# Kernel optimization log

Hardware: AMD Instinct MI355X
Metric: run time of the kernel (lower is better)

## Reference

```python
import jax, jax.numpy as jnp
import numpy as np

N = 50000      # nodes
E = 800000     # edges (before self-loops)
F_IN = 256
H = 4          # heads
C1 = 128
C2 = 64
NCLS = 50
NEG_SLOPE = 0.2


def setup_inputs() -> dict:
    key = jax.random.key(0)
    ks = jax.random.split(key, 12)
    x = jax.random.normal(ks[0], (N, F_IN), dtype=jnp.float32)
    edge_index = jax.random.randint(ks[1], (2, E), 0, N, dtype=jnp.int32)
    s1 = 1.0 / np.sqrt(F_IN)
    s2 = 1.0 / np.sqrt(H * C1)
    s3 = 1.0 / np.sqrt(H * C2)
    return {
        "x": x,
        "edge_index": edge_index,
        "W1": jax.random.normal(ks[2], (F_IN, H * C1), dtype=jnp.float32) * s1,
        "a_src1": jax.random.normal(ks[3], (H, C1), dtype=jnp.float32) * s2,
        "a_dst1": jax.random.normal(ks[4], (H, C1), dtype=jnp.float32) * s2,
        "b1": jnp.zeros((H * C1,), dtype=jnp.float32),
        "W2": jax.random.normal(ks[5], (H * C1, H * C2), dtype=jnp.float32) * s2,
        "a_src2": jax.random.normal(ks[6], (H, C2), dtype=jnp.float32) * s3,
        "a_dst2": jax.random.normal(ks[7], (H, C2), dtype=jnp.float32) * s3,
        "b2": jnp.zeros((H * C2,), dtype=jnp.float32),
        "Wf": jax.random.normal(ks[8], (H * C2, NCLS), dtype=jnp.float32) * s3,
        "bf": jnp.zeros((NCLS,), dtype=jnp.float32),
    }


def _gat_conv(x, src, dst, W, a_src, a_dst, b, heads, ch):
    # h: [N, H, C] transformed features
    h = (x @ W).reshape(N, heads, ch)
    # per-node attention halves (standard GAT decomposition, avoids per-edge d-dim gather for scores)
    asrc = jnp.sum(h * a_src[None], axis=-1)  # [N, H]
    adst = jnp.sum(h * a_dst[None], axis=-1)  # [N, H]
    e = jax.nn.leaky_relu(asrc[src] + adst[dst], NEG_SLOPE)  # [E, H]
    # softmax over edges sharing the same destination node
    m = jax.ops.segment_max(e, dst, num_segments=N)          # [N, H]
    ex = jnp.exp(e - m[dst])
    denom = jax.ops.segment_sum(ex, dst, num_segments=N)     # [N, H]
    alpha = ex / (denom[dst] + 1e-16)                        # [E, H]
    msg = h[src] * alpha[:, :, None]                         # [E, H, C]
    out = jax.ops.segment_sum(msg, dst, num_segments=N)      # [N, H, C]
    return out.reshape(N, heads * ch) + b


def reference(x, edge_index, W1, a_src1, a_dst1, b1, W2, a_src2, a_dst2, b2, Wf, bf):
    # PyG GATConv adds self-loops by default
    loops = jnp.arange(N, dtype=edge_index.dtype)
    src = jnp.concatenate([edge_index[0], loops])
    dst = jnp.concatenate([edge_index[1], loops])
    h = _gat_conv(x, src, dst, W1, a_src1, a_dst1, b1, H, C1)
    h = jax.nn.elu(h)
    # F.dropout is identity in eval mode
    h = _gat_conv(h, src, dst, W2, a_src2, a_dst2, b2, H, C2)
    h = jax.nn.elu(h)
    return h @ Wf + bf
```

## Files before the change

kernel.cpp:

```cpp
#include <hip/hip_runtime.h>
#include <hip/hip_bf16.h>
#include <cmath>

#define NN 50000
#define EE 800000
#define ET 850000
#define HH 4
#define CC1 128
#define CC2 64
#define FIN 256
#define NCLS 50

typedef __attribute__((ext_vector_type(8))) short   short8;
typedef __attribute__((ext_vector_type(8))) unsigned short ushort8;
typedef __attribute__((ext_vector_type(4))) unsigned short ushortx4;
typedef __attribute__((ext_vector_type(4))) float   floatx4;

__device__ __forceinline__ unsigned short f2bf(float f) {
    union { float f; unsigned int u; } x; x.f = f;
    unsigned int lsb = (x.u >> 16) & 1u;
    x.u += 0x7fffu + lsb;
    return (unsigned short)(x.u >> 16);
}
__device__ __forceinline__ float bf2f(unsigned short b) {
    union { unsigned int u; float f; } x; x.u = ((unsigned int)b) << 16;
    return x.f;
}

typedef const __attribute__((address_space(1))) unsigned int* glds_gp_t;
typedef __attribute__((address_space(3))) unsigned int* glds_lp_t;
__device__ __forceinline__ void glds16(const void* g, void* l) {
    __builtin_amdgcn_global_load_lds((glds_gp_t)g, (glds_lp_t)l, 16, 0, 0);
}

__global__ __launch_bounds__(256) void cast_bf16(
    const float* __restrict__ in, unsigned short* __restrict__ out, int n4)
{
    int t = blockIdx.x * blockDim.x + threadIdx.x;
    if (t >= n4) return;
    float4 v = *(const float4*)(in + 4 * (size_t)t);
    unsigned short r0 = f2bf(v.x), r1 = f2bf(v.y), r2 = f2bf(v.z), r3 = f2bf(v.w);
    unsigned int lo = (unsigned int)r0 | ((unsigned int)r1 << 16);
    unsigned int hi = (unsigned int)r2 | ((unsigned int)r3 << 16);
    *(uint2*)(out + 4 * (size_t)t) = make_uint2(lo, hi);
}

__global__ __launch_bounds__(256) void transpose_cast(
    const float* __restrict__ W, unsigned short* __restrict__ Wt, int K, int N)
{
    int t = blockIdx.x * blockDim.x + threadIdx.x;
    if (t >= K * N) return;
    int n = t / K, k = t - n * K;
    Wt[t] = f2bf(W[(size_t)k * N + n]);
}

__global__ __launch_bounds__(256) void transpose_cast_pad(
    const float* __restrict__ W, unsigned short* __restrict__ Wt,
    int K, int N, int Npad)
{
    int t = blockIdx.x * blockDim.x + threadIdx.x;
    if (t >= K * Npad) return;
    int n = t / K, k = t - n * K;
    Wt[t] = (n < N) ? f2bf(W[(size_t)k * N + n]) : (unsigned short)0;
}

__global__ __launch_bounds__(256) void gemm_bf16_v2(
    const unsigned short* __restrict__ A,
    const unsigned short* __restrict__ Bt,
    unsigned short* __restrict__ C,
    int M, int N, int K)
{
    __shared__ unsigned short As[128 * 32];
    __shared__ unsigned short Bs[128 * 32];
    int tid = threadIdx.x, wave = tid >> 6, lane = tid & 63;
    int wm = (wave >> 1) * 64, wn = (wave & 1) * 64;
    int row0 = blockIdx.x * 128, col0 = blockIdx.y * 128;
    int lm = lane & 15, lq = lane >> 4, kq = lq * 8;
    floatx4 acc[4][4] = {};

    int srow = wave * 32 + (lane >> 2);
    int skk  = (lane & 3) * 8;
    int gra0 = row0 + srow;      if (gra0 >= M) gra0 = M - 1;
    int gra1 = row0 + srow + 16; if (gra1 >= M) gra1 = M - 1;
    const unsigned short* ga0 = A + (size_t)gra0 * K + skk;
    const unsigned short* ga1 = A + (size_t)gra1 * K + skk;
    const unsigned short* gb0 = Bt + (size_t)(col0 + srow) * K + skk;
    const unsigned short* gb1 = Bt + (size_t)(col0 + srow + 16) * K + skk;
    unsigned short* la0 = &As[(wave * 32) * 32];
    unsigned short* la1 = &As[(wave * 32 + 16) * 32];
    unsigned short* lb0 = &Bs[(wave * 32) * 32];
    unsigned short* lb1 = &Bs[(wave * 32 + 16) * 32];

    for (int k0 = 0; k0 < K; k0 += 32) {
        __syncthreads();
        glds16(ga0 + k0, la0);
        glds16(ga1 + k0, la1);
        glds16(gb0 + k0, lb0);
        glds16(gb1 + k0, lb1);
        __syncthreads();

        short8 af[4], bfr[4];
        #pragma unroll
        for (int mt = 0; mt < 4; ++mt)
            af[mt] = *(const short8*)&As[(wm + mt * 16 + lm) * 32 + kq];
        #pragma unroll
        for (int nt = 0; nt < 4; ++nt)
            bfr[nt] = *(const short8*)&Bs[(wn + nt * 16 + lm) * 32 + kq];
        #pragma unroll
        for (int mt = 0; mt < 4; ++mt)
            #pragma unroll
            for (int nt = 0; nt < 4; ++nt)
                acc[mt][nt] = __builtin_amdgcn_mfma_f32_16x16x32_bf16(
                    af[mt], bfr[nt], acc[mt][nt], 0, 0, 0);
    }

    #pragma unroll
    for (int mt = 0; mt < 4; ++mt) {
        int rbase = row0 + wm + mt * 16 + lq * 4;
        #pragma unroll
        for (int nt = 0; nt < 4; ++nt) {
            int c = col0 + wn + nt * 16 + lm;
            #pragma unroll
            for (int r = 0; r < 4; ++r) {
                int gr = rbase + r;
                if (gr < M) C[(size_t)gr * N + c] = f2bf(acc[mt][nt][r]);
            }
        }
    }
}

__global__ __launch_bounds__(128) void gemm_final(
    const unsigned short* __restrict__ A,
    const unsigned short* __restrict__ Bt,
    const float* __restrict__ bias,
    float* __restrict__ out, int M)
{
    __shared__ unsigned short As[128 * 40];
    __shared__ unsigned short Bs[64 * 40];
    int tid = threadIdx.x, wave = tid >> 6, lane = tid & 63;
    int row0 = blockIdx.x * 128;
    int lm = lane & 15, lq = lane >> 4, kq = lq * 8;
    floatx4 acc[4][4] = {};

    for (int k0 = 0; k0 < 256; k0 += 32) {
        int gr = row0 + tid; if (gr >= M) gr = M - 1;
        const unsigned short* ap = A + (size_t)gr * 256 + k0;
        ushort8 a0 = *(const ushort8*)ap;
        ushort8 a1 = *(const ushort8*)(ap + 8);
        ushort8 a2 = *(const ushort8*)(ap + 16);
        ushort8 a3 = *(const ushort8*)(ap + 24);
        const unsigned short* bp = Bt + (size_t)(tid >> 1) * 256 + k0 + (tid & 1) * 16;
        ushort8 b0 = *(const ushort8*)bp;
        ushort8 b1 = *(const ushort8*)(bp + 8);
        __syncthreads();
        *(ushort8*)&As[tid * 40 + 0]  = a0;
        *(ushort8*)&As[tid * 40 + 8]  = a1;
        *(ushort8*)&As[tid * 40 + 16] = a2;
        *(ushort8*)&As[tid * 40 + 24] = a3;
        *(ushort8*)&Bs[(tid >> 1) * 40 + (tid & 1) * 16]     = b0;
        *(ushort8*)&Bs[(tid >> 1) * 40 + (tid & 1) * 16 + 8] = b1;
        __syncthreads();

        short8 af[4], bfr[4];
        #pragma unroll
        for (int mt = 0; mt < 4; ++mt)
            af[mt] = *(const short8*)&As[(wave * 64 + mt * 16 + lm) * 40 + kq];
        #pragma unroll
        for (int nt = 0; nt < 4; ++nt)
            bfr[nt] = *(const short8*)&Bs[(nt * 16 + lm) * 40 + kq];
        #pragma unroll
        for (int mt = 0; mt < 4; ++mt)
            #pragma unroll
            for (int nt = 0; nt < 4; ++nt)
                acc[mt][nt] = __builtin_amdgcn_mfma_f32_16x16x32_bf16(
                    af[mt], bfr[nt], acc[mt][nt], 0, 0, 0);
    }

    #pragma unroll
    for (int mt = 0; mt < 4; ++mt) {
        int rbase = row0 + wave * 64 + mt * 16 + lq * 4;
        #pragma unroll
        for (int nt = 0; nt < 4; ++nt) {
            int c = nt * 16 + lm;
            if (c >= NCLS) continue;
            float bv = bias[c];
            #pragma unroll
            for (int r = 0; r < 4; ++r) {
                int gr = rbase + r;
                if (gr < M) out[(size_t)gr * NCLS + c] = acc[mt][nt][r] + bv;
            }
        }
    }
}

template<int C>
__global__ __launch_bounds__(256) void attn_scores2(
    const unsigned short* __restrict__ h, const float* __restrict__ a_src,
    const float* __restrict__ a_dst, float* __restrict__ asrc,
    float* __restrict__ adst)
{
    constexpr int HC = HH * C;
    constexpr int CPL = HC / 64;
    int wave = threadIdx.x >> 6;
    int lane = threadIdx.x & 63;
    int n = blockIdx.x * 4 + wave;
    if (n >= NN) return;
    int c0 = lane * CPL;
    int head = c0 / C;
    const unsigned short* hp = h + (size_t)n * HC + c0;
    float hv[CPL];
    if (CPL == 8) {
        ushort8 u = *(const ushort8*)hp;
        #pragma unroll
        for (int c = 0; c < 8; ++c) hv[c] = bf2f(u[c]);
    } else {
        ushortx4 u = *(const ushortx4*)hp;
        #pragma unroll
        for (int c = 0; c < 4; ++c) hv[c] = bf2f(u[c]);
    }
    float s1 = 0.f, s2 = 0.f;
    #pragma unroll
    for (int c = 0; c < CPL; ++c) {
        s1 += hv[c] * a_src[c0 + c];
        s2 += hv[c] * a_dst[c0 + c];
    }
    #pragma unroll
    for (int o = 8; o > 0; o >>= 1) {
        s1 += __shfl_xor(s1, o, 64);
        s2 += __shfl_xor(s2, o, 64);
    }
    if ((lane & 15) == 0) {
        asrc[n * HH + head] = s1;
        adst[n * HH + head] = s2;
    }
}

__global__ void edge_histogram(const int* __restrict__ ei, int* __restrict__ deg)
{
    int t = blockIdx.x * blockDim.x + threadIdx.x;
    if (t >= ET) return;
    int dst = (t < EE) ? ei[EE + t] : (t - EE);
    atomicAdd(&deg[dst], 1);
}

__global__ __launch_bounds__(256) void scan_reduce(
    const int* __restrict__ deg, int* __restrict__ partials)
{
    int i0 = blockIdx.x * 2048 + threadIdx.x * 8;
    int s = 0;
    #pragma unroll
    for (int k = 0; k < 8; ++k) { int i = i0 + k; s += (i < NN) ? deg[i] : 0; }
    #pragma unroll
    for (int o = 32; o > 0; o >>= 1) s += __shfl_xor(s, o, 64);
    __shared__ int ws[4];
    int lane = threadIdx.x & 63, wid = threadIdx.x >> 6;
    if (lane == 0) ws[wid] = s;
    __syncthreads();
    if (threadIdx.x == 0) partials[blockIdx.x] = ws[0] + ws[1] + ws[2] + ws[3];
}

__global__ __launch_bounds__(64) void scan_partials(int* __restrict__ partials, int nb)
{
    int lane = threadIdx.x;
    int v = (lane < nb) ? partials[lane] : 0;
    int s = v;
    #pragma unroll
    for (int o = 1; o < 64; o <<= 1) {
        int t = __shfl_up(s, o, 64);
        if (lane >= o) s += t;
    }
    if (lane < nb) partials[lane] = s - v;
}

__global__ __launch_bounds__(256) void scan_apply(
    const int* __restrict__ deg, const int* __restrict__ partials,
    int* __restrict__ off, int* __restrict__ pos)
{
    int i0 = blockIdx.x * 2048 + threadIdx.x * 8;
    int v[8]; int s = 0;
    #pragma unroll
    for (int k = 0; k < 8; ++k) {
        int i = i0 + k;
        v[k] = (i < NN) ? deg[i] : 0;
        s += v[k];
    }
    int lane = threadIdx.x & 63, wid = threadIdx.x >> 6;
    int sc = s;
    #pragma unroll
    for (int o = 1; o < 64; o <<= 1) {
        int t = __shfl_up(sc, o, 64);
        if (lane >= o) sc += t;
    }
    __shared__ int ws[4];
    if (lane == 63) ws[wid] = sc;
    __syncthreads();
    int woff = partials[blockIdx.x];
    for (int w = 0; w < wid; ++w) woff += ws[w];
    int excl = woff + sc - s;
    #pragma unroll
    for (int k = 0; k < 8; ++k) {
        int i = i0 + k;
        if (i < NN) { off[i] = excl; pos[i] = excl; }
        excl += v[k];
    }
    if (blockIdx.x == 0 && threadIdx.x == 0) off[NN] = ET;
}

__global__ void edge_scatter2(const int* __restrict__ ei,
                              int* __restrict__ pos,
                              int* __restrict__ csr_src,
                              int* __restrict__ csr_dst)
{
    int t = blockIdx.x * blockDim.x + threadIdx.x;
    if (t >= ET) return;
    int src, dst;
    if (t < EE) { src = ei[t]; dst = ei[EE + t]; }
    else        { src = t - EE; dst = t - EE; }
    int p = atomicAdd(&pos[dst], 1);
    csr_src[p] = src;
    csr_dst[p] = dst;
}

__global__ __launch_bounds__(256) void edge_scores(
    const int* __restrict__ csr_src, const int* __restrict__ csr_dst,
    const float* __restrict__ asrc, const float* __restrict__ adst,
    float4* __restrict__ exf)
{
    int t = blockIdx.x * blockDim.x + threadIdx.x;
    if (t >= ET) return;
    int s = csr_src[t];
    int d = csr_dst[t];
    float4 a = *(const float4*)(asrc + (size_t)s * HH);
    float4 b = *(const float4*)(adst + (size_t)d * HH);
    float e0 = a.x + b.x; e0 = e0 > 0.f ? e0 : 0.2f * e0;
    float e1 = a.y + b.y; e1 = e1 > 0.f ? e1 : 0.2f * e1;
    float e2 = a.z + b.z; e2 = e2 > 0.f ? e2 : 0.2f * e2;
    float e3 = a.w + b.w; e3 = e3 > 0.f ? e3 : 0.2f * e3;
    exf[t] = make_float4(__expf(e0), __expf(e1), __expf(e2), __expf(e3));
}

template<int C>
__global__ __launch_bounds__(256) void aggregate6(
    const unsigned short* __restrict__ h, const int* __restrict__ off,
    const int* __restrict__ csr_src, const float4* __restrict__ exf,
    const float* __restrict__ bias, unsigned short* __restrict__ outb)
{
    constexpr int HC = HH * C;
    constexpr int LPE = HC / 8;
    constexpr int EPW = 64 / LPE;
    constexpr int UNR = 8;
    __shared__ float exlds_all[4][64 * HH];
    int wave = threadIdx.x >> 6;
    int lane = threadIdx.x & 63;
    int n = blockIdx.x * 4 + wave;
    if (n >= NN) return;
    float* exlds = exlds_all[wave];
    int el  = (EPW == 1) ? 0 : (lane >> 5);
    int lel = (EPW == 1) ? lane : (lane & 31);
    int coff = lel * 8;
    int hl = coff / C;

    int start = off[n], end = off[n + 1];
    float dh0 = 0.f, dh1 = 0.f, dh2 = 0.f, dh3 = 0.f;
    float acc[8] = {0.f, 0.f, 0.f, 0.f, 0.f, 0.f, 0.f, 0.f};

    for (int cb = start; cb < end; cb += 64) {
        int eidx = cb + lane;
        bool valid = eidx < end;
        int s_lane = csr_src[valid ? eidx : end - 1];
        float4 xv = valid ? exf[eidx] : make_float4(0.f, 0.f, 0.f, 0.f);
        dh0 += xv.x; dh1 += xv.y; dh2 += xv.z; dh3 += xv.w;
        *(float4*)&exlds[lane * 4] = xv;

        int cnt = end - cb; if (cnt > 64) cnt = 64;
        int jmax = (cnt + UNR * EPW - 1) & ~(UNR * EPW - 1);
        for (int jj = 0; jj < jmax; jj += UNR * EPW) {
            int sidx[UNR]; float xs[UNR]; ushort8 uv[UNR];
            #pragma unroll
            for (int u = 0; u < UNR; ++u) {
                int e_lo = jj + u * EPW;
                if (EPW == 1) {
                    sidx[u] = __builtin_amdgcn_readlane(s_lane, e_lo);
                } else {
                    int sa = __builtin_amdgcn_readlane(s_lane, e_lo);
                    int sb = __builtin_amdgcn_readlane(s_lane, e_lo + 1);
                    sidx[u] = el ? sb : sa;
                }
                uv[u] = *(const ushort8*)(h + (size_t)sidx[u] * HC + coff);
                xs[u] = exlds[(e_lo + el) * 4 + hl];
            }
            #pragma unroll
            for (int u = 0; u < UNR; ++u)
                #pragma unroll
                for (int c = 0; c < 8; ++c)
                    acc[c] += xs[u] * bf2f(uv[u][c]);
        }
    }

    #pragma unroll
    for (int o = 32; o > 0; o >>= 1) {
        dh0 += __shfl_xor(dh0, o, 64);
        dh1 += __shfl_xor(dh1, o, 64);
        dh2 += __shfl_xor(dh2, o, 64);
        dh3 += __shfl_xor(dh3, o, 64);
    }
    if (EPW == 2) {
        #pragma unroll
        for (int c = 0; c < 8; ++c)
            acc[c] += __shfl_xor(acc[c], 32, 64);
    }
    float d = (hl == 0) ? dh0 : (hl == 1) ? dh1 : (hl == 2) ? dh2 : dh3;
    float inv = 1.f / (d + 1e-16f);
    if (el == 0) {
        float4 b0 = *(const float4*)(bias + coff);
        float4 b1 = *(const float4*)(bias + coff + 4);
        float bb[8] = {b0.x, b0.y, b0.z, b0.w, b1.x, b1.y, b1.z, b1.w};
        unsigned int pk[4];
        #pragma unroll
        for (int c2 = 0; c2 < 4; ++c2) {
            float ua = acc[2 * c2]     * inv + bb[2 * c2];
            float ub = acc[2 * c2 + 1] * inv + bb[2 * c2 + 1];
            ua = ua > 0.f ? ua : expm1f(ua);
            ub = ub > 0.f ? ub : expm1f(ub);
            pk[c2] = (unsigned int)f2bf(ua) | ((unsigned int)f2bf(ub) << 16);
        }
        *(uint4*)(outb + (size_t)n * HC + coff) = make_uint4(pk[0], pk[1], pk[2], pk[3]);
    }
}

extern "C" void kernel_launch(void* const* d_in, const int* in_sizes, int n_in,
                              void* d_out, int out_size, void* d_ws, size_t ws_size,
                              hipStream_t stream) {
    const float* x      = (const float*)d_in[0];
    const int*   ei     = (const int*)d_in[1];
    const float* W1     = (const float*)d_in[2];
    const float* a_src1 = (const float*)d_in[3];
    const float* a_dst1 = (const float*)d_in[4];
    const float* b1     = (const float*)d_in[5];
    const float* W2     = (const float*)d_in[6];
    const float* a_src2 = (const float*)d_in[7];
    const float* a_dst2 = (const float*)d_in[8];
    const float* b2     = (const float*)d_in[9];
    const float* Wf     = (const float*)d_in[10];
    const float* bf     = (const float*)d_in[11];
    float* out = (float*)d_out;

    char* p = (char*)d_ws;
    unsigned short* xb    = (unsigned short*)p; p += (size_t)NN * FIN * 2;
    unsigned short* h1b   = (unsigned short*)p; p += (size_t)NN * HH * CC1 * 2;
    unsigned short* out1b = (unsigned short*)p; p += (size_t)NN * HH * CC1 * 2;
    unsigned short* h2b   = (unsigned short*)p; p += (size_t)NN * HH * CC2 * 2;
    unsigned short* out2b = (unsigned short*)p; p += (size_t)NN * HH * CC2 * 2;
    unsigned short* W1t   = (unsigned short*)p; p += (size_t)FIN * HH * CC1 * 2;
    unsigned short* W2t   = (unsigned short*)p; p += (size_t)HH * CC1 * HH * CC2 * 2;
    unsigned short* Wft   = (unsigned short*)p; p += (size_t)64 * HH * CC2 * 2;
    float* asrc           = (float*)p;          p += (size_t)NN * HH * 4;
    float* adst           = (float*)p;          p += (size_t)NN * HH * 4;
    float4* exf           = (float4*)p;         p += (size_t)ET * 16;
    int* deg              = (int*)p;            p += (size_t)NN * 4;
    int* csr_off          = (int*)p;            p += (size_t)(NN + 1) * 4 + 12;
    int* csr_pos          = (int*)p;            p += (size_t)NN * 4;
    int* csr_src          = (int*)p;            p += (size_t)ET * 4;
    int* csr_dst          = (int*)p;            p += (size_t)ET * 4;
    int* partials         = (int*)p;            p += 64 * 4;

    hipMemsetAsync(deg, 0, NN * sizeof(int), stream);

    cast_bf16<<<(NN * FIN / 4 + 255) / 256, 256, 0, stream>>>(x, xb, NN * FIN / 4);
    transpose_cast<<<(FIN * HH * CC1 + 255) / 256, 256, 0, stream>>>(W1, W1t, FIN, HH * CC1);
    transpose_cast<<<(HH * CC1 * HH * CC2 + 255) / 256, 256, 0, stream>>>(W2, W2t, HH * CC1, HH * CC2);
    transpose_cast_pad<<<(HH * CC2 * 64 + 255) / 256, 256, 0, stream>>>(Wf, Wft, HH * CC2, NCLS, 64);

    const int NB = (NN + 2047) / 2048;
    edge_histogram<<<(ET + 255) / 256, 256, 0, stream>>>(ei, deg);
    scan_reduce<<<NB, 256, 0, stream>>>(deg, partials);
    scan_partials<<<1, 64, 0, stream>>>(partials, NB);
    scan_apply<<<NB, 256, 0, stream>>>(deg, partials, csr_off, csr_pos);
    edge_scatter2<<<(ET + 255) / 256, 256, 0, stream>>>(ei, csr_pos, csr_src, csr_dst);

    gemm_bf16_v2<<<dim3((NN + 127) / 128, (HH * CC1) / 128), 256, 0, stream>>>(
        xb, W1t, h1b, NN, HH * CC1, FIN);
    attn_scores2<CC1><<<(NN + 3) / 4, 256, 0, stream>>>(h1b, a_src1, a_dst1, asrc, adst);
    edge_scores<<<(ET + 255) / 256, 256, 0, stream>>>(csr_src, csr_dst, asrc, adst, exf);
    aggregate6<CC1><<<(NN + 3) / 4, 256, 0, stream>>>(h1b, csr_off, csr_src, exf, b1, out1b);

    gemm_bf16_v2<<<dim3((NN + 127) / 128, (HH * CC2) / 128), 256, 0, stream>>>(
        out1b, W2t, h2b, NN, HH * CC2, HH * CC1);
    attn_scores2<CC2><<<(NN + 3) / 4, 256, 0, stream>>>(h2b, a_src2, a_dst2, asrc, adst);
    edge_scores<<<(ET + 255) / 256, 256, 0, stream>>>(csr_src, csr_dst, asrc, adst, exf);
    aggregate6<CC2><<<(NN + 3) / 4, 256, 0, stream>>>(h2b, csr_off, csr_src, exf, b2, out2b);

    gemm_final<<<(NN + 127) / 128, 128, 0, stream>>>(out2b, Wft, bf, out, NN);
}
```

Before: 526.2 us.

## Fuse attention-score reductions into GEMM epilogue and merge prep kernels

Computes per-node attention halves (asrc/adst) in the GEMM epilogue from fp32 accumulators via wave shuffles and atomicAdd, removing the separate attn_scores pass that re-reads h. Merges the bf16 cast and three weight transpose kernels into one launch, and folds the partial-scan kernel into scan_apply. The workspace is reordered so asrc, adst and deg are zeroed with one memset, and asrc/adst are cleared again before layer 2. This adds atomics and extra memsets, and scores now come from unrounded fp32 rather than the bf16-rounded h.

```diff
diff --git a/kernel.cpp b/kernel.cpp
--- a/kernel.cpp
+++ b/kernel.cpp
@@ -33,41 +33,47 @@
     __builtin_amdgcn_global_load_lds((glds_gp_t)g, (glds_lp_t)l, 16, 0, 0);
 }
 
-__global__ __launch_bounds__(256) void cast_bf16(
-    const float* __restrict__ in, unsigned short* __restrict__ out, int n4)
-{
-    int t = blockIdx.x * blockDim.x + threadIdx.x;
-    if (t >= n4) return;
-    float4 v = *(const float4*)(in + 4 * (size_t)t);
-    unsigned short r0 = f2bf(v.x), r1 = f2bf(v.y), r2 = f2bf(v.z), r3 = f2bf(v.w);
-    unsigned int lo = (unsigned int)r0 | ((unsigned int)r1 << 16);
-    unsigned int hi = (unsigned int)r2 | ((unsigned int)r3 << 16);
-    *(uint2*)(out + 4 * (size_t)t) = make_uint2(lo, hi);
-}
-
-__global__ __launch_bounds__(256) void transpose_cast(
-    const float* __restrict__ W, unsigned short* __restrict__ Wt, int K, int N)
-{
-    int t = blockIdx.x * blockDim.x + threadIdx.x;
-    if (t >= K * N) return;
-    int n = t / K, k = t - n * K;
-    Wt[t] = f2bf(W[(size_t)k * N + n]);
-}
-
-__global__ __launch_bounds__(256) void transpose_cast_pad(
-    const float* __restrict__ W, unsigned short* __restrict__ Wt,
-    int K, int N, int Npad)
-{
-    int t = blockIdx.x * blockDim.x + threadIdx.x;
-    if (t >= K * Npad) return;
-    int n = t / K, k = t - n * K;
-    Wt[t] = (n < N) ? f2bf(W[(size_t)k * N + n]) : (unsigned short)0;
-}
-
-__global__ __launch_bounds__(256) void gemm_bf16_v2(
+#define NB_CAST 12500
+#define NB_W1   512
+#define NB_W2   512
+#define NB_WF   64
+__global__ __launch_bounds__(256) void prep_fused(
+    const float* __restrict__ x, unsigned short* __restrict__ xb,
+    const float* __restrict__ W1, unsigned short* __restrict__ W1t,
+    const float* __restrict__ W2, unsigned short* __restrict__ W2t,
+    const float* __restrict__ Wf, unsigned short* __restrict__ Wft)
+{
+    int b = blockIdx.x;
+    if (b < NB_CAST) {
+        int t = b * 256 + threadIdx.x;
+        float4 v = *(const float4*)(x + 4 * (size_t)t);
+        unsigned int lo = (unsigned int)f2bf(v.x) | ((unsigned int)f2bf(v.y) << 16);
+        unsigned int hi = (unsigned int)f2bf(v.z) | ((unsigned int)f2bf(v.w) << 16);
+        *(uint2*)(xb + 4 * (size_t)t) = make_uint2(lo, hi);
+    } else if (b < NB_CAST + NB_W1) {
+        int t = (b - NB_CAST) * 256 + threadIdx.x;
+        int n = t >> 8, k = t & 255;
+        W1t[t] = f2bf(W1[(size_t)k * 512 + n]);
+    } else if (b < NB_CAST + NB_W1 + NB_W2) {
+        int t = (b - NB_CAST - NB_W1) * 256 + threadIdx.x;
+        int n = t >> 9, k = t & 511;
+        W2t[t] = f2bf(W2[(size_t)k * 256 + n]);
+    } else {
+        int t = (b - NB_CAST - NB_W1 - NB_W2) * 256 + threadIdx.x;
+        int n = t >> 8, k = t & 255;
+        Wft[t] = (n < NCLS) ? f2bf(Wf[(size_t)k * NCLS + n]) : (unsigned short)0;
+    }
+}
+
+template<int HSH>
+__global__ __launch_bounds__(256) void gemm_bf16_v3(
     const unsigned short* __restrict__ A,
     const unsigned short* __restrict__ Bt,
     unsigned short* __restrict__ C,
+    const float* __restrict__ a_src_full,
+    const float* __restrict__ a_dst_full,
+    float* __restrict__ asrc,
+    float* __restrict__ adst,
     int M, int N, int K)
 {
     __shared__ unsigned short As[128 * 32];
@@ -124,6 +130,35 @@
             for (int r = 0; r < 4; ++r) {
                 int gr = rbase + r;
                 if (gr < M) C[(size_t)gr * N + c] = f2bf(acc[mt][nt][r]);
+            }
+        }
+    }
+
+    float asw[4], adw[4];
+    #pragma unroll
+    for (int nt = 0; nt < 4; ++nt) {
+        int c = col0 + wn + nt * 16 + lm;
+        asw[nt] = a_src_full[c];
+        adw[nt] = a_dst_full[c];
+    }
+    int head = (col0 + wn) >> HSH;
+    #pragma unroll
+    for (int mt = 0; mt < 4; ++mt) {
+        #pragma unroll
+        for (int r = 0; r < 4; ++r) {
+            float s1 = acc[mt][0][r] * asw[0] + acc[mt][1][r] * asw[1]
+                     + acc[mt][2][r] * asw[2] + acc[mt][3][r] * asw[3];
+            float s2 = acc[mt][0][r] * adw[0] + acc[mt][1][r] * adw[1]
+                     + acc[mt][2][r] * adw[2] + acc[mt][3][r] * adw[3];
+            #pragma unroll
+            for (int o = 1; o < 16; o <<= 1) {
+                s1 += __shfl_xor(s1, o, 64);
+                s2 += __shfl_xor(s2, o, 64);
+            }
+            int row = row0 + wm + mt * 16 + lq * 4 + r;
+            if (lm == 0 && row < M) {
+                atomicAdd(&asrc[row * HH + head], s1);
+                atomicAdd(&adst[row * HH + head], s2);
             }
         }
     }
@@ -193,48 +228,6 @@
     }
 }
 
-template<int C>
-__global__ __launch_bounds__(256) void attn_scores2(
-    const unsigned short* __restrict__ h, const float* __restrict__ a_src,
-    const float* __restrict__ a_dst, float* __restrict__ asrc,
-    float* __restrict__ adst)
-{
-    constexpr int HC = HH * C;
-    constexpr int CPL = HC / 64;
-    int wave = threadIdx.x >> 6;
-    int lane = threadIdx.x & 63;
-    int n = blockIdx.x * 4 + wave;
-    if (n >= NN) return;
-    int c0 = lane * CPL;
-    int head = c0 / C;
-    const unsigned short* hp = h + (size_t)n * HC + c0;
-    float hv[CPL];
-    if (CPL == 8) {
-        ushort8 u = *(const ushort8*)hp;
-        #pragma unroll
-        for (int c = 0; c < 8; ++c) hv[c] = bf2f(u[c]);
-    } else {
-        ushortx4 u = *(const ushortx4*)hp;
-        #pragma unroll
-        for (int c = 0; c < 4; ++c) hv[c] = bf2f(u[c]);
-    }
-    float s1 = 0.f, s2 = 0.f;
-    #pragma unroll
-    for (int c = 0; c < CPL; ++c) {
-        s1 += hv[c] * a_src[c0 + c];
-        s2 += hv[c] * a_dst[c0 + c];
-    }
-    #pragma unroll
-    for (int o = 8; o > 0; o >>= 1) {
-        s1 += __shfl_xor(s1, o, 64);
-        s2 += __shfl_xor(s2, o, 64);
-    }
-    if ((lane & 15) == 0) {
-        asrc[n * HH + head] = s1;
-        adst[n * HH + head] = s2;
-    }
-}
-
 __global__ void edge_histogram(const int* __restrict__ ei, int* __restrict__ deg)
 {
     int t = blockIdx.x * blockDim.x + threadIdx.x;
@@ -259,23 +252,25 @@
     if (threadIdx.x == 0) partials[blockIdx.x] = ws[0] + ws[1] + ws[2] + ws[3];
 }
 
-__global__ __launch_bounds__(64) void scan_partials(int* __restrict__ partials, int nb)
-{
-    int lane = threadIdx.x;
-    int v = (lane < nb) ? partials[lane] : 0;
-    int s = v;
-    #pragma unroll
-    for (int o = 1; o < 64; o <<= 1) {
-        int t = __shfl_up(s, o, 64);
-        if (lane >= o) s += t;
-    }
-    if (lane < nb) partials[lane] = s - v;
-}
-
+#define SCAN_NB 25
 __global__ __launch_bounds__(256) void scan_apply(
     const int* __restrict__ deg, const int* __restrict__ partials,
     int* __restrict__ off, int* __restrict__ pos)
 {
+    __shared__ int spE[SCAN_NB];
+    __shared__ int ws[4];
+    int lane = threadIdx.x & 63, wid = threadIdx.x >> 6;
+    if (wid == 0) {
+        int v = (lane < SCAN_NB) ? partials[lane] : 0;
+        int s = v;
+        #pragma unroll
+        for (int o = 1; o < 32; o <<= 1) {
+            int t = __shfl_up(s, o, 64);
+            if (lane >= o) s += t;
+        }
+        if (lane < SCAN_NB) spE[lane] = s - v;
+    }
+
     int i0 = blockIdx.x * 2048 + threadIdx.x * 8;
     int v[8]; int s = 0;
     #pragma unroll
@@ -284,17 +279,15 @@
         v[k] = (i < NN) ? deg[i] : 0;
         s += v[k];
     }
-    int lane = threadIdx.x & 63, wid = threadIdx.x >> 6;
     int sc = s;
     #pragma unroll
     for (int o = 1; o < 64; o <<= 1) {
         int t = __shfl_up(sc, o, 64);
         if (lane >= o) sc += t;
     }
-    __shared__ int ws[4];
     if (lane == 63) ws[wid] = sc;
     __syncthreads();
-    int woff = partials[blockIdx.x];
+    int woff = spE[blockIdx.x];
     for (int w = 0; w < wid; ++w) woff += ws[w];
     int excl = woff + sc - s;
     #pragma unroll
@@ -454,9 +447,9 @@
     unsigned short* W1t   = (unsigned short*)p; p += (size_t)FIN * HH * CC1 * 2;
     unsigned short* W2t   = (unsigned short*)p; p += (size_t)HH * CC1 * HH * CC2 * 2;
     unsigned short* Wft   = (unsigned short*)p; p += (size_t)64 * HH * CC2 * 2;
+    float4* exf           = (float4*)p;         p += (size_t)ET * 16;
     float* asrc           = (float*)p;          p += (size_t)NN * HH * 4;
     float* adst           = (float*)p;          p += (size_t)NN * HH * 4;
-    float4* exf           = (float4*)p;         p += (size_t)ET * 16;
     int* deg              = (int*)p;            p += (size_t)NN * 4;
     int* csr_off          = (int*)p;            p += (size_t)(NN + 1) * 4 + 12;
     int* csr_pos          = (int*)p;            p += (size_t)NN * 4;
@@ -464,29 +457,25 @@
     int* csr_dst          = (int*)p;            p += (size_t)ET * 4;
     int* partials         = (int*)p;            p += 64 * 4;
 
-    hipMemsetAsync(deg, 0, NN * sizeof(int), stream);
-
-    cast_bf16<<<(NN * FIN / 4 + 255) / 256, 256, 0, stream>>>(x, xb, NN * FIN / 4);
-    transpose_cast<<<(FIN * HH * CC1 + 255) / 256, 256, 0, stream>>>(W1, W1t, FIN, HH * CC1);
-    transpose_cast<<<(HH * CC1 * HH * CC2 + 255) / 256, 256, 0, stream>>>(W2, W2t, HH * CC1, HH * CC2);
-    transpose_cast_pad<<<(HH * CC2 * 64 + 255) / 256, 256, 0, stream>>>(Wf, Wft, HH * CC2, NCLS, 64);
-
-    const int NB = (NN + 2047) / 2048;
+    hipMemsetAsync(asrc, 0, (size_t)(NN * HH * 2 + NN) * 4, stream);
+
+    prep_fused<<<NB_CAST + NB_W1 + NB_W2 + NB_WF, 256, 0, stream>>>(
+        x, xb, W1, W1t, W2, W2t, Wf, Wft);
+
     edge_histogram<<<(ET + 255) / 256, 256, 0, stream>>>(ei, deg);
-    scan_reduce<<<NB, 256, 0, stream>>>(deg, partials);
-    scan_partials<<<1, 64, 0, stream>>>(partials, NB);
-    scan_apply<<<NB, 256, 0, stream>>>(deg, partials, csr_off, csr_pos);
+    scan_reduce<<<SCAN_NB, 256, 0, stream>>>(deg, partials);
+    scan_apply<<<SCAN_NB, 256, 0, stream>>>(deg, partials, csr_off, csr_pos);
     edge_scatter2<<<(ET + 255) / 256, 256, 0, stream>>>(ei, csr_pos, csr_src, csr_dst);
 
-    gemm_bf16_v2<<<dim3((NN + 127) / 128, (HH * CC1) / 128), 256, 0, stream>>>(
-        xb, W1t, h1b, NN, HH * CC1, FIN);
-    attn_scores2<CC1><<<(NN + 3) / 4, 256, 0, stream>>>(h1b, a_src1, a_dst1, asrc, adst);
+    gemm_bf16_v3<7><<<dim3((NN + 127) / 128, (HH * CC1) / 128), 256, 0, stream>>>(
+        xb, W1t, h1b, a_src1, a_dst1, asrc, adst, NN, HH * CC1, FIN);
     edge_scores<<<(ET + 255) / 256, 256, 0, stream>>>(csr_src, csr_dst, asrc, adst, exf);
     aggregate6<CC1><<<(NN + 3) / 4, 256, 0, stream>>>(h1b, csr_off, csr_src, exf, b1, out1b);
 
-    gemm_bf16_v2<<<dim3((NN + 127) / 128, (HH * CC2) / 128), 256, 0, stream>>>(
-        out1b, W2t, h2b, NN, HH * CC2, HH * CC1);
-    attn_scores2<CC2><<<(NN + 3) / 4, 256, 0, stream>>>(h2b, a_src2, a_dst2, asrc, adst);
+    hipMemsetAsync(asrc, 0, (size_t)NN * HH * 2 * 4, stream);
+
+    gemm_bf16_v3<6><<<dim3((NN + 127) / 128, (HH * CC2) / 128), 256, 0, stream>>>(
+        out1b, W2t, h2b, a_src2, a_dst2, asrc, adst, NN, HH * CC2, HH * CC1);
     edge_scores<<<(ET + 255) / 256, 256, 0, stream>>>(csr_src, csr_dst, asrc, adst, exf);
     aggregate6<CC2><<<(NN + 3) / 4, 256, 0, stream>>>(h2b, csr_off, csr_src, exf, b2, out2b);
 
```

Result: slower. 552.6 us (+5.0%).
